# Performance work log

Measured on AMD Instinct MI355X. Metric: run time of the kernel, lower is better.

Reference implementation:

```python
import jax, jax.numpy as jnp
import numpy as np


def _interpn_linear(vol, loc):
    """Trilinear interpolation matching voxelmorph/neuron interpn.
    vol: [X, Y, Z, C]; loc: [X, Y, Z, 3] absolute sample coordinates.
    """
    spatial = vol.shape[:-1]
    ndims = len(spatial)
    max_f = jnp.asarray([d - 1 for d in spatial], dtype=loc.dtype)
    max_i = jnp.asarray([d - 1 for d in spatial], dtype=jnp.int32)

    loc = jnp.clip(loc, 0.0, max_f)          # clipped_loc
    loc0 = jnp.floor(loc)
    loc0i = jnp.clip(loc0.astype(jnp.int32), 0, max_i)
    loc1i = jnp.clip(loc0i + 1, 0, max_i)

    # voxelmorph weights: corner-0 weight = loc1 - clipped_loc, corner-1 = 1 - that
    w_lo = loc1i.astype(loc.dtype) - loc      # weight for taking loc0
    w_hi = 1.0 - w_lo                          # weight for taking loc1

    out = jnp.zeros(vol.shape, vol.dtype)
    for c in range(2 ** ndims):
        bits = [(c >> d) & 1 for d in range(ndims)]
        idx = tuple(jnp.where(bits[d], loc1i[..., d], loc0i[..., d]) if False else (loc1i[..., d] if bits[d] else loc0i[..., d]) for d in range(ndims))
        w = jnp.ones(loc.shape[:-1], loc.dtype)
        for d in range(ndims):
            w = w * (w_hi[..., d] if bits[d] else w_lo[..., d])
        out = out + vol[idx] * w[..., None]
    return out


def setup_inputs() -> dict:
    key = jax.random.key(0)
    k1, k2 = jax.random.split(key)
    vol = jax.random.normal(k1, (2, 160, 160, 160, 1), dtype=jnp.float32)
    flow = jax.random.normal(k2, (2, 160, 160, 160, 3), dtype=jnp.float32)
    return {"vol": vol, "flow": flow}


def reference(vol, flow):
    # dense displacement field: absolute location = identity grid + flow
    spatial = vol.shape[1:-1]
    grid = jnp.stack(
        jnp.meshgrid(*[jnp.arange(d, dtype=flow.dtype) for d in spatial], indexing="ij"),
        axis=-1,
    )  # [X,Y,Z,3]
    loc = grid[None] + flow  # [B,X,Y,Z,3]
    return jax.vmap(_interpn_linear)(vol, loc)
```

## Files before the change

### kernel.cpp

```cpp
#include <hip/hip_runtime.h>


typedef float f32x4 __attribute__((ext_vector_type(4)));
typedef float f32x2 __attribute__((ext_vector_type(2), aligned(4)));

#define DIM 160
#define DD  (DIM * DIM)
#define DDD (DIM * DIM * DIM)
#define BATCH 2
#define BLK 256
#define NBX 40
#define NBY 40
#define NBZ 10
#define NBLK (BATCH * NBX * NBY * NBZ)
#define CHUNK (NBLK / 8)

#define FROW 52

__global__ __launch_bounds__(256) void st_warp_kernel(
    const float* __restrict__ vol,
    const float* __restrict__ flow,
    float* __restrict__ out)
{
    __shared__ float sflow[16 * FROW];
    __shared__ float sout[BLK];

    int tid = threadIdx.x;
    int bid = blockIdx.x;
    int swz = (bid & 7) * CHUNK + (bid >> 3);

    int bb = swz / (NBX * NBY * NBZ);
    int r  = swz - bb * (NBX * NBY * NBZ);
    int xb = r / (NBY * NBZ);
    int r2 = r - xb * (NBY * NBZ);
    int yb = r2 / NBZ;
    int zb = r2 - yb * NBZ;

    int x0b = xb * 4, y0b = yb * 4, z0b = zb * 16;

    if (tid < 192) {
        int rr = tid / 12;
        int q  = tid - rr * 12;
        int xr = x0b + (rr >> 2);
        int yr = y0b + (rr & 3);
        const f32x4* src = (const f32x4*)(flow +
            ((size_t)((bb * DIM + xr) * DIM + yr) * DIM + z0b) * 3);
        f32x4 v = __builtin_nontemporal_load(&src[q]);
        *(f32x4*)&sflow[rr * FROW + q * 4] = v;
    }
    __syncthreads();

    int lx  = (tid >> 4) & 3;
    int ly  = (tid >> 2) & 3;
    int lz  = ((tid >> 6) << 2) | (tid & 3);
    int row = (lx << 2) | ly;

    float fx = sflow[row * FROW + lz * 3 + 0];
    float fy = sflow[row * FROW + lz * 3 + 1];
    float fz = sflow[row * FROW + lz * 3 + 2];

    int x = x0b + lx, y = y0b + ly, z = z0b + lz;

    const float maxf = (float)(DIM - 1);

    float lxf = fminf(fmaxf((float)x + fx, 0.0f), maxf);
    float lyf = fminf(fmaxf((float)y + fy, 0.0f), maxf);
    float lzf = fminf(fmaxf((float)z + fz, 0.0f), maxf);

    int x0 = (int)floorf(lxf);
    int y0 = (int)floorf(lyf);
    int z0 = (int)floorf(lzf);
    x0 = min(max(x0, 0), DIM - 1);
    y0 = min(max(y0, 0), DIM - 1);
    z0 = min(max(z0, 0), DIM - 1);

    int x1 = min(x0 + 1, DIM - 1);
    int y1 = min(y0 + 1, DIM - 1);
    int z1 = min(z0 + 1, DIM - 1);

    float wx0 = (float)x1 - lxf;  float wx1 = 1.0f - wx0;
    float wy0 = (float)y1 - lyf;  float wy1 = 1.0f - wy0;
    float wz0 = (float)z1 - lzf;  float wz1 = 1.0f - wz0;

    const float* vb = vol + (size_t)bb * DDD;
    int bx0 = x0 * DD, bx1 = x1 * DD;
    int by0 = y0 * DIM, by1 = y1 * DIM;

    int zp = min(z0, DIM - 2);
    f32x2 p00 = *(const f32x2*)(vb + bx0 + by0 + zp);
    f32x2 p10 = *(const f32x2*)(vb + bx1 + by0 + zp);
    f32x2 p01 = *(const f32x2*)(vb + bx0 + by1 + zp);
    f32x2 p11 = *(const f32x2*)(vb + bx1 + by1 + zp);

    float acc;
    acc  = p00.x * (wx0 * wy0 * wz0);
    acc += p10.x * (wx1 * wy0 * wz0);
    acc += p01.x * (wx0 * wy1 * wz0);
    acc += p11.x * (wx1 * wy1 * wz0);
    acc += p00.y * (wx0 * wy0 * wz1);
    acc += p10.y * (wx1 * wy0 * wz1);
    acc += p01.y * (wx0 * wy1 * wz1);
    acc += p11.y * (wx1 * wy1 * wz1);

    sout[tid] = acc;
    __syncthreads();

    int ro = tid >> 4;
    int zo = tid & 15;
    int tsrc = ((zo >> 2) << 6) | ((ro >> 2) << 4) | ((ro & 3) << 2) | (zo & 3);
    int xs = x0b + (ro >> 2);
    int ys = y0b + (ro & 3);
    float v = sout[tsrc];
    __builtin_nontemporal_store(v,
        &out[(size_t)((bb * DIM + xs) * DIM + ys) * DIM + z0b + zo]);
}

extern "C" void kernel_launch(void* const* d_in, const int* in_sizes, int n_in,
                              void* d_out, int out_size, void* d_ws, size_t ws_size,
                              hipStream_t stream)
{
    const float* vol  = (const float*)d_in[0];
    const float* flow = (const float*)d_in[1];
    float* out = (float*)d_out;

    st_warp_kernel<<<NBLK, BLK, 0, stream>>>(vol, flow, out);
}
```

Measured before the change: 202.7 us.

## Process two z-voxels per thread with 4x4x32 tiles and vectorized stores

Doubles each block's tile along z to 32, so every thread computes two output voxels and the grid has half as many blocks. All eight gather loads for both voxels are issued before any arithmetic to raise memory-level parallelism. The interpolation is refactored into a separable FMA form, the redundant floor and clamps are dropped because coordinates are already non-negative, and output goes through padded shared memory as float2 nontemporal stores. The trade-off is higher register pressure and more flow data loaded per block.

```diff
diff --git a/kernel.cpp b/kernel.cpp
--- a/kernel.cpp
+++ b/kernel.cpp
@@ -2,20 +2,22 @@
 
 
 typedef float f32x4 __attribute__((ext_vector_type(4)));
-typedef float f32x2 __attribute__((ext_vector_type(2), aligned(4)));
+typedef float f32x2u __attribute__((ext_vector_type(2), aligned(4)));
+typedef float f32x2 __attribute__((ext_vector_type(2)));
 
 #define DIM 160
 #define DD  (DIM * DIM)
 #define DDD (DIM * DIM * DIM)
-#define BATCH 2
 #define BLK 256
 #define NBX 40
 #define NBY 40
-#define NBZ 10
-#define NBLK (BATCH * NBX * NBY * NBZ)
+#define NBZ 5
+#define TPB (NBX * NBY * NBZ)
+#define NBLK (2 * TPB)
 #define CHUNK (NBLK / 8)
 
-#define FROW 52
+#define FROW 100
+#define SOROW 34
 
 __global__ __launch_bounds__(256) void st_warp_kernel(
     const float* __restrict__ vol,
@@ -23,26 +25,33 @@
     float* __restrict__ out)
 {
     __shared__ float sflow[16 * FROW];
-    __shared__ float sout[BLK];
+    __shared__ float sout[16 * SOROW];
 
     int tid = threadIdx.x;
     int bid = blockIdx.x;
     int swz = (bid & 7) * CHUNK + (bid >> 3);
 
-    int bb = swz / (NBX * NBY * NBZ);
-    int r  = swz - bb * (NBX * NBY * NBZ);
+    int bb = swz / TPB;
+    int r  = swz - bb * TPB;
     int xb = r / (NBY * NBZ);
     int r2 = r - xb * (NBY * NBZ);
     int yb = r2 / NBZ;
     int zb = r2 - yb * NBZ;
 
-    int x0b = xb * 4, y0b = yb * 4, z0b = zb * 16;
+    int x0b = xb << 2, y0b = yb << 2, z0b = zb << 5;
 
-    if (tid < 192) {
-        int rr = tid / 12;
-        int q  = tid - rr * 12;
-        int xr = x0b + (rr >> 2);
-        int yr = y0b + (rr & 3);
+    {
+        int rr = tid / 24, q = tid - rr * 24;
+        int xr = x0b + (rr >> 2), yr = y0b + (rr & 3);
+        const f32x4* src = (const f32x4*)(flow +
+            ((size_t)((bb * DIM + xr) * DIM + yr) * DIM + z0b) * 3);
+        f32x4 v = __builtin_nontemporal_load(&src[q]);
+        *(f32x4*)&sflow[rr * FROW + q * 4] = v;
+    }
+    if (tid < 128) {
+        int i  = tid + 256;
+        int rr = i / 24, q = i - rr * 24;
+        int xr = x0b + (rr >> 2), yr = y0b + (rr & 3);
         const f32x4* src = (const f32x4*)(flow +
             ((size_t)((bb * DIM + xr) * DIM + yr) * DIM + z0b) * 3);
         f32x4 v = __builtin_nontemporal_load(&src[q]);
@@ -52,67 +61,67 @@
 
     int lx  = (tid >> 4) & 3;
     int ly  = (tid >> 2) & 3;
-    int lz  = ((tid >> 6) << 2) | (tid & 3);
+    int lzA = ((tid >> 6) << 2) | (tid & 3);
     int row = (lx << 2) | ly;
 
-    float fx = sflow[row * FROW + lz * 3 + 0];
-    float fy = sflow[row * FROW + lz * 3 + 1];
-    float fz = sflow[row * FROW + lz * 3 + 2];
-
-    int x = x0b + lx, y = y0b + ly, z = z0b + lz;
-
+    int x = x0b + lx, y = y0b + ly;
+    const float* vb = vol + (size_t)bb * DDD;
     const float maxf = (float)(DIM - 1);
 
-    float lxf = fminf(fmaxf((float)x + fx, 0.0f), maxf);
-    float lyf = fminf(fmaxf((float)y + fy, 0.0f), maxf);
-    float lzf = fminf(fmaxf((float)z + fz, 0.0f), maxf);
+    float wx0[2], wx1[2], wy0[2], wy1[2], wz0[2], wz1[2];
+    f32x2u p00[2], p10[2], p01[2], p11[2];
+#pragma unroll
+    for (int h = 0; h < 2; ++h) {
+        int lz = lzA + h * 16;
+        float fx = sflow[row * FROW + lz * 3 + 0];
+        float fy = sflow[row * FROW + lz * 3 + 1];
+        float fz = sflow[row * FROW + lz * 3 + 2];
 
-    int x0 = (int)floorf(lxf);
-    int y0 = (int)floorf(lyf);
-    int z0 = (int)floorf(lzf);
-    x0 = min(max(x0, 0), DIM - 1);
-    y0 = min(max(y0, 0), DIM - 1);
-    z0 = min(max(z0, 0), DIM - 1);
+        float lxf = fminf(fmaxf((float)x + fx, 0.0f), maxf);
+        float lyf = fminf(fmaxf((float)y + fy, 0.0f), maxf);
+        float lzf = fminf(fmaxf((float)(z0b + lz) + fz, 0.0f), maxf);
 
-    int x1 = min(x0 + 1, DIM - 1);
-    int y1 = min(y0 + 1, DIM - 1);
-    int z1 = min(z0 + 1, DIM - 1);
+        int x0 = (int)lxf;
+        int y0 = (int)lyf;
+        int z0 = (int)lzf;
+        int x1 = min(x0 + 1, DIM - 1);
+        int y1 = min(y0 + 1, DIM - 1);
+        int z1 = min(z0 + 1, DIM - 1);
 
-    float wx0 = (float)x1 - lxf;  float wx1 = 1.0f - wx0;
-    float wy0 = (float)y1 - lyf;  float wy1 = 1.0f - wy0;
-    float wz0 = (float)z1 - lzf;  float wz1 = 1.0f - wz0;
+        wx0[h] = (float)x1 - lxf;  wx1[h] = 1.0f - wx0[h];
+        wy0[h] = (float)y1 - lyf;  wy1[h] = 1.0f - wy0[h];
+        wz0[h] = (float)z1 - lzf;  wz1[h] = 1.0f - wz0[h];
 
-    const float* vb = vol + (size_t)bb * DDD;
-    int bx0 = x0 * DD, bx1 = x1 * DD;
-    int by0 = y0 * DIM, by1 = y1 * DIM;
+        int zp  = min(z0, DIM - 2);
+        int a00 = x0 * DD + y0 * DIM + zp;
+        int dx  = (x1 - x0) * DD;
+        int dy  = (y1 - y0) * DIM;
+        p00[h] = *(const f32x2u*)(vb + a00);
+        p10[h] = *(const f32x2u*)(vb + a00 + dx);
+        p01[h] = *(const f32x2u*)(vb + a00 + dy);
+        p11[h] = *(const f32x2u*)(vb + a00 + dx + dy);
+    }
 
-    int zp = min(z0, DIM - 2);
-    f32x2 p00 = *(const f32x2*)(vb + bx0 + by0 + zp);
-    f32x2 p10 = *(const f32x2*)(vb + bx1 + by0 + zp);
-    f32x2 p01 = *(const f32x2*)(vb + bx0 + by1 + zp);
-    f32x2 p11 = *(const f32x2*)(vb + bx1 + by1 + zp);
-
-    float acc;
-    acc  = p00.x * (wx0 * wy0 * wz0);
-    acc += p10.x * (wx1 * wy0 * wz0);
-    acc += p01.x * (wx0 * wy1 * wz0);
-    acc += p11.x * (wx1 * wy1 * wz0);
-    acc += p00.y * (wx0 * wy0 * wz1);
-    acc += p10.y * (wx1 * wy0 * wz1);
-    acc += p01.y * (wx0 * wy1 * wz1);
-    acc += p11.y * (wx1 * wy1 * wz1);
-
-    sout[tid] = acc;
+#pragma unroll
+    for (int h = 0; h < 2; ++h) {
+        float t00 = fmaf(wz1[h], p00[h].y, wz0[h] * p00[h].x);
+        float t10 = fmaf(wz1[h], p10[h].y, wz0[h] * p10[h].x);
+        float t01 = fmaf(wz1[h], p01[h].y, wz0[h] * p01[h].x);
+        float t11 = fmaf(wz1[h], p11[h].y, wz0[h] * p11[h].x);
+        float s0  = fmaf(wy1[h], t01, wy0[h] * t00);
+        float s1  = fmaf(wy1[h], t11, wy0[h] * t10);
+        float acc = fmaf(wx1[h], s1, wx0[h] * s0);
+        sout[row * SOROW + lzA + h * 16] = acc;
+    }
     __syncthreads();
 
     int ro = tid >> 4;
-    int zo = tid & 15;
-    int tsrc = ((zo >> 2) << 6) | ((ro >> 2) << 4) | ((ro & 3) << 2) | (zo & 3);
+    int j  = tid & 15;
+    f32x2 v2 = *(const f32x2*)&sout[ro * SOROW + 2 * j];
     int xs = x0b + (ro >> 2);
     int ys = y0b + (ro & 3);
-    float v = sout[tsrc];
-    __builtin_nontemporal_store(v,
-        &out[(size_t)((bb * DIM + xs) * DIM + ys) * DIM + z0b + zo]);
+    __builtin_nontemporal_store(v2,
+        (f32x2*)&out[(size_t)((bb * DIM + xs) * DIM + ys) * DIM + z0b + 2 * j]);
 }
 
 extern "C" void kernel_launch(void* const* d_in, const int* in_sizes, int n_in,
```

After: 196.6 us. -3.0%, faster.
